# Optimization experiments

Measured on AMD Instinct MI355X. Metric: run time of the kernel, lower is better.

## Reference

```python
import jax, jax.numpy as jnp
import numpy as np

D_MODEL, HEADS, D_FF = 1024, 16, 4096
D_K = D_MODEL // HEADS
EPS = 1e-5


def layer_norm(x, g, b):
    mu = jnp.mean(x, axis=-1, keepdims=True)
    var = jnp.mean((x - mu) ** 2, axis=-1, keepdims=True)
    return (x - mu) * jax.lax.rsqrt(var + EPS) * g + b


def setup_inputs() -> dict:
    key = jax.random.key(0)
    ks = jax.random.split(key, 16)
    B, S = 2, 2048
    s = 0.02
    return {
        "src": jax.random.normal(ks[0], (B, S, D_MODEL), jnp.float32),
        "corr": jax.random.normal(ks[1], (B, S, S), jnp.float32),
        "pos": jax.random.normal(ks[2], (B, S, D_MODEL), jnp.float32),
        "Wq": jax.random.normal(ks[3], (D_MODEL, D_MODEL), jnp.float32) * s,
        "bq": jnp.zeros((D_MODEL,), jnp.float32),
        "Wk": jax.random.normal(ks[4], (D_MODEL, D_MODEL), jnp.float32) * s,
        "bk": jnp.zeros((D_MODEL,), jnp.float32),
        "Wv": jax.random.normal(ks[5], (D_MODEL, D_MODEL), jnp.float32) * s,
        "bv": jnp.zeros((D_MODEL,), jnp.float32),
        "Wo": jax.random.normal(ks[6], (D_MODEL, D_MODEL), jnp.float32) * s,
        "bo": jnp.zeros((D_MODEL,), jnp.float32),
        "W1": jax.random.normal(ks[7], (D_MODEL, D_FF), jnp.float32) * s,
        "b1": jnp.zeros((D_FF,), jnp.float32),
        "W2": jax.random.normal(ks[8], (D_FF, D_MODEL), jnp.float32) * s,
        "b2": jnp.zeros((D_MODEL,), jnp.float32),
        "g1": jnp.ones((D_MODEL,), jnp.float32),
        "be1": jnp.zeros((D_MODEL,), jnp.float32),
        "g2": jnp.ones((D_MODEL,), jnp.float32),
        "be2": jnp.zeros((D_MODEL,), jnp.float32),
    }


def reference(src, corr, pos, Wq, bq, Wk, bk, Wv, bv, Wo, bo, W1, b1, W2, b2, g1, be1, g2, be2):
    B, S, _ = src.shape
    qk_in = src + pos  # with_pos_embed for q and k; value uses raw src
    # QKV projections -> [B, H, S, d_k]
    def split_heads(x):
        return x.reshape(B, S, HEADS, D_K).transpose(0, 2, 1, 3)
    q = split_heads(qk_in @ Wq + bq)
    k = split_heads(qk_in @ Wk + bk)
    v = split_heads(src @ Wv + bv)
    # scores [B, H, S, S] with additive correlation bias before softmax
    scores = jnp.einsum("bhqd,bhkd->bhqk", q, k) / jnp.sqrt(jnp.float32(D_K))
    scores = scores + corr[:, None, :, :]
    attn = jax.nn.softmax(scores, axis=-1)
    ctx = jnp.einsum("bhqk,bhkd->bhqd", attn, v)
    concat = ctx.transpose(0, 2, 1, 3).reshape(B, S, D_MODEL)
    attn_out = concat @ Wo + bo
    # post-norm residual blocks (dropout = identity in eval)
    x = layer_norm(src + attn_out, g1, be1)
    ffn = jax.nn.relu(x @ W1 + b1) @ W2 + b2
    x = layer_norm(x + ffn, g2, be2)
    return x
```

## Files before the change

kernel.cpp:

```cpp
#include <hip/hip_runtime.h>
#include <hip/hip_bf16.h>

#define S_LEN  2048
#define BATCH  2
#define DMODEL 1024
#define NHEAD  16
#define DHEAD  64
#define DFF    4096
#define NTOK   (BATCH * S_LEN)
#define QKVLD  3072
#define NSPLIT 2

typedef __attribute__((ext_vector_type(8))) short short8;
typedef __attribute__((ext_vector_type(4))) short short4v;
typedef __attribute__((ext_vector_type(4))) float f32x4;

__device__ __forceinline__ short f2bs(float f) {
  __hip_bfloat16 h = __float2bfloat16(f);
  short s;
  __builtin_memcpy(&s, &h, sizeof(short));
  return s;
}

__device__ __forceinline__ float bs2f(short s) {
  unsigned u = ((unsigned)(unsigned short)s) << 16;
  float f;
  __builtin_memcpy(&f, &u, sizeof(float));
  return f;
}

__device__ __forceinline__ f32x4 mfma16(short8 a, short8 b, f32x4 c) {
  return __builtin_amdgcn_mfma_f32_16x16x32_bf16(a, b, c, 0, 0, 0);
}

__device__ __forceinline__ void load_lds16(const short* g, short* l) {
  __builtin_amdgcn_global_load_lds(
      (const __attribute__((address_space(1))) void*)g,
      (__attribute__((address_space(3))) void*)l, 16, 0, 0);
}

__global__ void transpose_cast(const float* __restrict__ in, short* __restrict__ out,
                               int R, int C, float scale) {
  __shared__ float tile[32][33];
  const int c0 = blockIdx.x * 32, r0 = blockIdx.y * 32;
  const int tx = threadIdx.x, ty = threadIdx.y;
#pragma unroll
  for (int i = 0; i < 32; i += 8)
    tile[ty + i][tx] = in[(size_t)(r0 + ty + i) * C + c0 + tx];
  __syncthreads();
#pragma unroll
  for (int i = 0; i < 32; i += 8)
    out[(size_t)(c0 + ty + i) * R + r0 + tx] = f2bs(tile[tx][ty + i] * scale);
}

__global__ __launch_bounds__(256) void transpose_bf16(
    const short* __restrict__ in, short* __restrict__ out, int R, int LDin) {
  __shared__ __attribute__((aligned(16))) short tile[64][72];
  const int c0 = blockIdx.x * 64, r0 = blockIdx.y * 64;
#pragma unroll
  for (int i = 0; i < 2; i++) {
    const int idx = threadIdx.x + 256 * i;
    const int rr = idx >> 3, cc8 = (idx & 7) * 8;
    *(int4*)(&tile[rr][cc8]) = *(const int4*)(in + (size_t)(r0 + rr) * LDin + c0 + cc8);
  }
  __syncthreads();
#pragma unroll
  for (int i = 0; i < 2; i++) {
    const int idx = threadIdx.x + 256 * i;
    const int rr = idx >> 3, cc8 = (idx & 7) * 8;
    short8 v;
#pragma unroll
    for (int j = 0; j < 8; j++) v[j] = tile[cc8 + j][rr];
    *(short8*)(out + (size_t)(c0 + rr) * R + r0 + cc8) = v;
  }
}

__global__ void concat_bias(const float* __restrict__ bq, const float* __restrict__ bk,
                            const float* __restrict__ bv, float* __restrict__ bqkv) {
  const int i = blockIdx.x * 256 + threadIdx.x;
  float v;
  if (i < DMODEL) v = bq[i] * 0.125f;
  else if (i < 2 * DMODEL) v = bk[i - DMODEL];
  else v = bv[i - 2 * DMODEL];
  bqkv[i] = v;
}

__global__ void prep_tokens(const float* __restrict__ src, const float* __restrict__ pos,
                            short* __restrict__ qkb, short* __restrict__ srcb) {
  const int i = (blockIdx.x * blockDim.x + threadIdx.x) * 4;
  float4 s = *(const float4*)(src + i);
  float4 p = *(const float4*)(pos + i);
  short4v q4 = {f2bs(s.x + p.x), f2bs(s.y + p.y), f2bs(s.z + p.z), f2bs(s.w + p.w)};
  short4v s4 = {f2bs(s.x), f2bs(s.y), f2bs(s.z), f2bs(s.w)};
  *(short4v*)(qkb + i) = q4;
  *(short4v*)(srcb + i) = s4;
}

__global__ void prep_corr(const float* __restrict__ corr, short* __restrict__ corrb) {
  const size_t i = ((size_t)blockIdx.x * 256 + threadIdx.x) * 4;
  float4 c = *(const float4*)(corr + i);
  short4v o = {f2bs(c.x), f2bs(c.y), f2bs(c.z), f2bs(c.w)};
  *(short4v*)(corrb + i) = o;
}

template <int RELU, int OUT_BF16>
__global__ __launch_bounds__(256) void gemm_bt(
    const short* __restrict__ A0, const short* __restrict__ A1,
    const short* __restrict__ Bt, const float* __restrict__ bias,
    float* __restrict__ Cf, short* __restrict__ Cb,
    int M, int N, int K, int splitcol) {
  __shared__ __attribute__((aligned(16))) short As[128 * 32];
  __shared__ __attribute__((aligned(16))) short Bs[128 * 32];

  const int tid = threadIdx.x;
  const int wave = tid >> 6, lane = tid & 63;
  const int lm = lane & 15, lq = lane >> 4;
  const int row0 = blockIdx.y * 128, col0 = blockIdx.x * 128;
  const int wr = (wave >> 1) * 64, wc = (wave & 1) * 64;

  const short* A = (col0 < splitcol) ? A0 : A1;
  const short* ag = A + (size_t)(row0 + wave * 32 + (lane >> 2)) * K + (lane & 3) * 8;
  const short* bg = Bt + (size_t)(col0 + wave * 32 + (lane >> 2)) * K + (lane & 3) * 8;
  short* asl = &As[wave * 32 * 32];
  short* bsl = &Bs[wave * 32 * 32];

  f32x4 acc[4][4];
#pragma unroll
  for (int i = 0; i < 4; i++)
#pragma unroll
    for (int j = 0; j < 4; j++) acc[i][j] = (f32x4){0.f, 0.f, 0.f, 0.f};

  for (int k0 = 0; k0 < K; k0 += 32) {
    load_lds16(ag + k0, asl);
    load_lds16(ag + (size_t)16 * K + k0, asl + 16 * 32);
    load_lds16(bg + k0, bsl);
    load_lds16(bg + (size_t)16 * K + k0, bsl + 16 * 32);
    __syncthreads();

    short8 af[4], bfr[4];
#pragma unroll
    for (int i = 0; i < 4; i++)
      af[i] = *(const short8*)(&As[(wr + 16 * i + lm) * 32 + lq * 8]);
#pragma unroll
    for (int j = 0; j < 4; j++)
      bfr[j] = *(const short8*)(&Bs[(wc + 16 * j + lm) * 32 + lq * 8]);
#pragma unroll
    for (int i = 0; i < 4; i++)
#pragma unroll
      for (int j = 0; j < 4; j++) acc[i][j] = mfma16(af[i], bfr[j], acc[i][j]);
    __syncthreads();
  }

#pragma unroll
  for (int i = 0; i < 4; i++) {
#pragma unroll
    for (int j = 0; j < 4; j++) {
      const int col = col0 + wc + 16 * j + lm;
      const float bs = bias[col];
#pragma unroll
      for (int r = 0; r < 4; r++) {
        const int row = row0 + wr + 16 * i + lq * 4 + r;
        float v = acc[i][j][r] + bs;
        if (RELU) v = fmaxf(v, 0.f);
        if (OUT_BF16)
          Cb[(size_t)row * N + col] = f2bs(v);
        else
          Cf[(size_t)row * N + col] = v;
      }
    }
  }
}

__global__ __launch_bounds__(256) void gemm_bt_part(
    const short* __restrict__ A, const short* __restrict__ Bt,
    float* __restrict__ Cf, int M, int N, int K, int Kslice) {
  __shared__ __attribute__((aligned(16))) short As[128 * 32];
  __shared__ __attribute__((aligned(16))) short Bs[128 * 32];

  const int tid = threadIdx.x;
  const int wave = tid >> 6, lane = tid & 63;
  const int lm = lane & 15, lq = lane >> 4;
  const int row0 = blockIdx.y * 128, col0 = blockIdx.x * 128;
  const int kbase = blockIdx.z * Kslice;
  const int wr = (wave >> 1) * 64, wc = (wave & 1) * 64;
  Cf += (size_t)blockIdx.z * M * N;

  const short* ag = A + (size_t)(row0 + wave * 32 + (lane >> 2)) * K + (lane & 3) * 8;
  const short* bg = Bt + (size_t)(col0 + wave * 32 + (lane >> 2)) * K + (lane & 3) * 8;
  short* asl = &As[wave * 32 * 32];
  short* bsl = &Bs[wave * 32 * 32];

  f32x4 acc[4][4];
#pragma unroll
  for (int i = 0; i < 4; i++)
#pragma unroll
    for (int j = 0; j < 4; j++) acc[i][j] = (f32x4){0.f, 0.f, 0.f, 0.f};

  for (int k0 = kbase; k0 < kbase + Kslice; k0 += 32) {
    load_lds16(ag + k0, asl);
    load_lds16(ag + (size_t)16 * K + k0, asl + 16 * 32);
    load_lds16(bg + k0, bsl);
    load_lds16(bg + (size_t)16 * K + k0, bsl + 16 * 32);
    __syncthreads();

    short8 af[4], bfr[4];
#pragma unroll
    for (int i = 0; i < 4; i++)
      af[i] = *(const short8*)(&As[(wr + 16 * i + lm) * 32 + lq * 8]);
#pragma unroll
    for (int j = 0; j < 4; j++)
      bfr[j] = *(const short8*)(&Bs[(wc + 16 * j + lm) * 32 + lq * 8]);
#pragma unroll
    for (int i = 0; i < 4; i++)
#pragma unroll
      for (int j = 0; j < 4; j++) acc[i][j] = mfma16(af[i], bfr[j], acc[i][j]);
    __syncthreads();
  }

#pragma unroll
  for (int i = 0; i < 4; i++) {
#pragma unroll
    for (int j = 0; j < 4; j++) {
      const int col = col0 + wc + 16 * j + lm;
#pragma unroll
      for (int r = 0; r < 4; r++) {
        const int row = row0 + wr + 16 * i + lq * 4 + r;
        Cf[(size_t)row * N + col] = acc[i][j][r];
      }
    }
  }
}

__global__ __launch_bounds__(512, 8) void attn_kernel(
    const short* __restrict__ QKV,
    const short* __restrict__ VT,
    const short* __restrict__ corrb,
    float* __restrict__ Op,
    float* __restrict__ lp) {
  const int h = blockIdx.x, qtile = blockIdx.y;
  const int b = blockIdx.z >> 1, split = blockIdx.z & 1;
  const int koff = split * (S_LEN / NSPLIT);
  const int tid = threadIdx.x;
  const int wave = tid >> 6, lane = tid & 63;
  const int lm = lane & 15, lq = lane >> 4;
  const int qb = qtile * 128 + wave * 16;
  const int fx = lm & 7;
  const int fy = (lm >> 1) & 3;

  __shared__ __attribute__((aligned(16))) short Ks[32 * 64];
  __shared__ __attribute__((aligned(16))) short Vs[64 * 32];
  __shared__ __attribute__((aligned(16))) short Ps[8 * 16 * 32];

  const short* q0 = QKV + (size_t)(b * S_LEN + qb + lm) * QKVLD + h * DHEAD;
  const short8 qA0 = *(const short8*)(q0 + lq * 8);
  const short8 qA1 = *(const short8*)(q0 + lq * 8 + 32);

  f32x4 oA[4];
#pragma unroll
  for (int t = 0; t < 4; t++) oA[t] = (f32x4){0.f, 0.f, 0.f, 0.f};
  f32x4 lacc = (f32x4){0.f, 0.f, 0.f, 0.f};

  const short* c0 = corrb + (size_t)(b * S_LEN + qb + lm) * S_LEN;

  const int st = tid & 255;
  const bool isK = tid < 256;
  short* sdst;
  const short* sgp;
  size_t sstep;
  if (isK) {
    const int krow = st >> 3, ku = st & 7;
    sdst = &Ks[krow * 64 + ((ku ^ (krow & 7)) * 8)];
    sgp = QKV + (size_t)(b * S_LEN + koff + krow) * QKVLD + DMODEL + h * DHEAD + ku * 8;
    sstep = (size_t)32 * QKVLD;
  } else {
    const int vrow = st >> 2, vu = st & 3;
    sdst = &Vs[vrow * 32 + ((vu ^ ((vrow >> 1) & 3)) * 8)];
    sgp = VT + (size_t)(h * DHEAD + vrow) * NTOK + b * S_LEN + koff + vu * 8;
    sstep = 32;
  }

  for (int kt = koff; kt < koff + S_LEN / NSPLIT; kt += 32) {
    *(int4*)sdst = *(const int4*)sgp;
    sgp += sstep;
    __syncthreads();

    f32x4 sv[2];
    __builtin_amdgcn_s_setprio(1);
#pragma unroll
    for (int t = 0; t < 2; t++) {
      const int rb = (t * 16 + lm) * 64;
      const short8 kf0 = *(const short8*)(&Ks[rb + (lq ^ fx) * 8]);
      const short8 kf1 = *(const short8*)(&Ks[rb + ((lq + 4) ^ fx) * 8]);
      f32x4 a = (f32x4){0.f, 0.f, 0.f, 0.f};
      a = mfma16(kf0, qA0, a);
      a = mfma16(kf1, qA1, a);
      sv[t] = a;
    }
    __builtin_amdgcn_s_setprio(0);

#pragma unroll
    for (int t = 0; t < 2; t++) {
      const short4v cr = *(const short4v*)(c0 + kt + t * 16 + lq * 4);
#pragma unroll
      for (int r = 0; r < 4; r++)
        sv[t][r] = __expf(sv[t][r] + bs2f(cr[r]));
      lacc += sv[t];
      short4v pA = {f2bs(sv[t][0]), f2bs(sv[t][1]), f2bs(sv[t][2]), f2bs(sv[t][3])};
      const int pu = ((2 * t + (lq >> 1)) ^ fy) * 8 + (lq & 1) * 4;
      *(short4v*)(&Ps[wave * 512 + lm * 32 + pu]) = pA;
    }

    const short8 pA0 = *(const short8*)(&Ps[wave * 512 + lm * 32 + (lq ^ fy) * 8]);
    __builtin_amdgcn_s_setprio(1);
#pragma unroll
    for (int t = 0; t < 4; t++) {
      const int vrb = (t * 16 + lm) * 32;
      const short8 vf0 = *(const short8*)(&Vs[vrb + (lq ^ fy) * 8]);
      oA[t] = mfma16(vf0, pA0, oA[t]);
    }
    __builtin_amdgcn_s_setprio(0);
    __syncthreads();
  }

  float lA = lacc[0] + lacc[1] + lacc[2] + lacc[3];
  lA += __shfl_xor(lA, 16);
  lA += __shfl_xor(lA, 32);
  if (lq == 0)
    lp[((size_t)split * NTOK + b * S_LEN + qb + lm) * NHEAD + h] = lA;
  float* opA = Op + (size_t)split * NTOK * DMODEL +
               (size_t)(b * S_LEN + qb + lm) * DMODEL + h * DHEAD;
#pragma unroll
  for (int t = 0; t < 4; t++)
    *(f32x4*)(opA + t * 16 + lq * 4) = oA[t];
}

__global__ __launch_bounds__(256) void combine_ctx(
    const float* __restrict__ Op, const float* __restrict__ lp,
    short* __restrict__ ctx) {
  const size_t idx = ((size_t)blockIdx.x * 256 + threadIdx.x) * 4;
  const int token = (int)(idx >> 10);
  const int d = (int)(idx & 1023);
  const int h = d >> 6;
  f32x4 o = (f32x4){0.f, 0.f, 0.f, 0.f};
  float l = 0.f;
#pragma unroll
  for (int s = 0; s < NSPLIT; s++) {
    o += *(const f32x4*)(Op + (size_t)s * NTOK * DMODEL + idx);
    l += lp[((size_t)s * NTOK + token) * NHEAD + h];
  }
  const float inv = 1.0f / l;
  short4v ov = {f2bs(o[0] * inv), f2bs(o[1] * inv),
                f2bs(o[2] * inv), f2bs(o[3] * inv)};
  *(short4v*)(ctx + idx) = ov;
}

__global__ __launch_bounds__(256) void residual_ln3(
    const float* __restrict__ xa, const float* __restrict__ p0,
    const float* __restrict__ p1, const float* __restrict__ bias,
    const float* __restrict__ g, const float* __restrict__ be,
    float* __restrict__ outf, short* __restrict__ outb) {
  const int row = blockIdx.x;
  const int t = threadIdx.x;
  const size_t base = (size_t)row * DMODEL + t * 4;
  float4 a = *(const float4*)(xa + base);
  f32x4 q0 = *(const f32x4*)(p0 + base);
  f32x4 q1 = *(const f32x4*)(p1 + base);
  f32x4 bb = *(const f32x4*)(bias + t * 4);
  const float v0 = a.x + q0[0] + q1[0] + bb[0];
  const float v1 = a.y + q0[1] + q1[1] + bb[1];
  const float v2 = a.z + q0[2] + q1[2] + bb[2];
  const float v3 = a.w + q0[3] + q1[3] + bb[3];
  float sum = v0 + v1 + v2 + v3;
  float sq = v0 * v0 + v1 * v1 + v2 * v2 + v3 * v3;
#pragma unroll
  for (int off = 1; off < 64; off <<= 1) {
    sum += __shfl_xor(sum, off);
    sq += __shfl_xor(sq, off);
  }
  __shared__ float ssum[4], ssq[4];
  const int wave = t >> 6;
  if ((t & 63) == 0) { ssum[wave] = sum; ssq[wave] = sq; }
  __syncthreads();
  sum = ssum[0] + ssum[1] + ssum[2] + ssum[3];
  sq = ssq[0] + ssq[1] + ssq[2] + ssq[3];
  const float mean = sum * (1.0f / DMODEL);
  const float var = sq * (1.0f / DMODEL) - mean * mean;
  const float rstd = rsqrtf(var + 1e-5f);
  float4 gv = *(const float4*)(g + t * 4);
  float4 bv = *(const float4*)(be + t * 4);
  const float o0 = (v0 - mean) * rstd * gv.x + bv.x;
  const float o1 = (v1 - mean) * rstd * gv.y + bv.y;
  const float o2 = (v2 - mean) * rstd * gv.z + bv.z;
  const float o3 = (v3 - mean) * rstd * gv.w + bv.w;
  if (outf) {
    float4 ov = {o0, o1, o2, o3};
    *(float4*)(outf + base) = ov;
  }
  if (outb) {
    short4v ob = {f2bs(o0), f2bs(o1), f2bs(o2), f2bs(o3)};
    *(short4v*)(outb + base) = ob;
  }
}

extern "C" void kernel_launch(void* const* d_in, const int* in_sizes, int n_in,
                              void* d_out, int out_size, void* d_ws, size_t ws_size,
                              hipStream_t stream) {
  const float* src = (const float*)d_in[0];
  const float* corr = (const float*)d_in[1];
  const float* pos = (const float*)d_in[2];
  const float* Wq = (const float*)d_in[3];
  const float* bq = (const float*)d_in[4];
  const float* Wk = (const float*)d_in[5];
  const float* bk = (const float*)d_in[6];
  const float* Wv = (const float*)d_in[7];
  const float* bv = (const float*)d_in[8];
  const float* Wo = (const float*)d_in[9];
  const float* bo = (const float*)d_in[10];
  const float* W1 = (const float*)d_in[11];
  const float* b1 = (const float*)d_in[12];
  const float* W2 = (const float*)d_in[13];
  const float* b2 = (const float*)d_in[14];
  const float* g1 = (const float*)d_in[15];
  const float* be1 = (const float*)d_in[16];
  const float* g2 = (const float*)d_in[17];
  const float* be2 = (const float*)d_in[18];
  float* out = (float*)d_out;

  char* ws = (char*)d_ws;
  size_t off = 0;
  auto alloc = [&](size_t bytes) {
    char* p = ws + off;
    off += (bytes + 255) & ~(size_t)255;
    return p;
  };
  short* WqkvT = (short*)alloc((size_t)QKVLD * DMODEL * 2);
  short* WoT = (short*)alloc((size_t)DMODEL * DMODEL * 2);
  short* W1T = (short*)alloc((size_t)DFF * DMODEL * 2);
  short* W2T = (short*)alloc((size_t)DMODEL * DFF * 2);
  float* bqkv = (float*)alloc((size_t)QKVLD * 4);
  short* qkb = (short*)alloc((size_t)NTOK * DMODEL * 2);
  short* srcb = (short*)alloc((size_t)NTOK * DMODEL * 2);
  short* QKVb = (short*)alloc((size_t)NTOK * QKVLD * 2);
  short* VTt = (short*)alloc((size_t)DMODEL * NTOK * 2);
  short* corrb = (short*)alloc((size_t)BATCH * S_LEN * S_LEN * 2);
  short* ctxb = (short*)alloc((size_t)NTOK * DMODEL * 2);
  float* lp = (float*)alloc((size_t)NSPLIT * NTOK * NHEAD * 4);
  float* Pp = (float*)alloc((size_t)2 * NTOK * DMODEL * 4);
  short* Hb = (short*)alloc((size_t)NTOK * DFF * 2);
  float* Op = Pp;
  float* x1f = (float*)alloc((size_t)NTOK * DMODEL * 4);
  short* x1b = (short*)alloc((size_t)NTOK * DMODEL * 2);

  const dim3 tb(32, 8);
  transpose_cast<<<dim3(32, 32), tb, 0, stream>>>(Wq, WqkvT, DMODEL, DMODEL, 0.125f);
  transpose_cast<<<dim3(32, 32), tb, 0, stream>>>(Wk, WqkvT + (size_t)DMODEL * DMODEL,
                                                  DMODEL, DMODEL, 1.0f);
  transpose_cast<<<dim3(32, 32), tb, 0, stream>>>(Wv, WqkvT + (size_t)2 * DMODEL * DMODEL,
                                                  DMODEL, DMODEL, 1.0f);
  transpose_cast<<<dim3(32, 32), tb, 0, stream>>>(Wo, WoT, DMODEL, DMODEL, 1.0f);
  transpose_cast<<<dim3(128, 32), tb, 0, stream>>>(W1, W1T, DMODEL, DFF, 1.0f);
  transpose_cast<<<dim3(32, 128), tb, 0, stream>>>(W2, W2T, DFF, DMODEL, 1.0f);
  concat_bias<<<QKVLD / 256, 256, 0, stream>>>(bq, bk, bv, bqkv);

  prep_tokens<<<(NTOK * DMODEL) / (256 * 4), 256, 0, stream>>>(src, pos, qkb, srcb);
  prep_corr<<<(BATCH * S_LEN * S_LEN) / (256 * 4), 256, 0, stream>>>(corr, corrb);

  gemm_bt<0, 1><<<dim3(QKVLD / 128, NTOK / 128), 256, 0, stream>>>(
      qkb, srcb, WqkvT, bqkv, nullptr, QKVb, NTOK, QKVLD, DMODEL, 2048);

  transpose_bf16<<<dim3(DMODEL / 64, NTOK / 64), 256, 0, stream>>>(
      QKVb + 2048, VTt, NTOK, QKVLD);

  attn_kernel<<<dim3(NHEAD, S_LEN / 128, BATCH * NSPLIT), 512, 0, stream>>>(
      QKVb, VTt, corrb, Op, lp);
  combine_ctx<<<(NTOK * DMODEL) / (256 * 4), 256, 0, stream>>>(Op, lp, ctxb);

  gemm_bt_part<<<dim3(DMODEL / 128, NTOK / 128, 2), 256, 0, stream>>>(
      ctxb, WoT, Pp, NTOK, DMODEL, DMODEL, DMODEL / 2);

  residual_ln3<<<NTOK, 256, 0, stream>>>(src, Pp, Pp + (size_t)NTOK * DMODEL,
                                         bo, g1, be1, x1f, x1b);

  gemm_bt<1, 1><<<dim3(DFF / 128, NTOK / 128), 256, 0, stream>>>(
      x1b, x1b, W1T, b1, nullptr, Hb, NTOK, DFF, DMODEL, 1 << 30);

  gemm_bt_part<<<dim3(DMODEL / 128, NTOK / 128, 2), 256, 0, stream>>>(
      Hb, W2T, Pp, NTOK, DMODEL, DFF, DFF / 2);

  residual_ln3<<<NTOK, 256, 0, stream>>>(x1f, Pp, Pp + (size_t)NTOK * DMODEL,
                                         b2, g2, be2, out, nullptr);
}
```

Before: 480.7 us.

## Drop split-K attention, fuse normalization into attention, merge prep kernels

Attention no longer splits the key range across two blocks. Each block now walks all 2048 keys and writes the normalized bf16 context directly, so the fp32 partial outputs and the combine_ctx kernel go away. The weight transposes and bias concat are merged into one launch, as are the token and corr casts, to cut launch overhead. The cost is half as many attention blocks (512 instead of 1024), which may leave the GPU less occupied, and each block runs a loop twice as long.

```diff
diff --git a/kernel.cpp b/kernel.cpp
--- a/kernel.cpp
+++ b/kernel.cpp
@@ -9,7 +9,6 @@
 #define DFF    4096
 #define NTOK   (BATCH * S_LEN)
 #define QKVLD  3072
-#define NSPLIT 2
 
 typedef __attribute__((ext_vector_type(8))) short short8;
 typedef __attribute__((ext_vector_type(4))) short short4v;
@@ -39,11 +38,48 @@
       (__attribute__((address_space(3))) void*)l, 16, 0, 0);
 }
 
-__global__ void transpose_cast(const float* __restrict__ in, short* __restrict__ out,
-                               int R, int C, float scale) {
+__global__ void prep_static(
+    const float* __restrict__ Wq, const float* __restrict__ Wk,
+    const float* __restrict__ Wv, const float* __restrict__ Wo,
+    const float* __restrict__ W1, const float* __restrict__ W2,
+    const float* __restrict__ bq, const float* __restrict__ bk,
+    const float* __restrict__ bv,
+    short* __restrict__ WqkvT, short* __restrict__ WoT,
+    short* __restrict__ W1T, short* __restrict__ W2T,
+    float* __restrict__ bqkv) {
+  const int gid = blockIdx.x;
+  const int tx = threadIdx.x, ty = threadIdx.y;
+
+  if (gid >= 12288) {
+    const int i = (gid - 12288) * 256 + ty * 32 + tx;
+    float v;
+    if (i < DMODEL) v = bq[i] * 0.125f;
+    else if (i < 2 * DMODEL) v = bk[i - DMODEL];
+    else v = bv[i - 2 * DMODEL];
+    bqkv[i] = v;
+    return;
+  }
+
+  const float* in;
+  short* out;
+  int R, C, t;
+  float scale = 1.0f;
+  if (gid < 4096) {
+    t = gid & 1023;
+    R = C = 1024;
+    if (gid < 1024)      { in = Wq; out = WqkvT;                 scale = 0.125f; }
+    else if (gid < 2048) { in = Wk; out = WqkvT + 1024 * 1024; }
+    else if (gid < 3072) { in = Wv; out = WqkvT + 2 * 1024 * 1024; }
+    else                 { in = Wo; out = WoT; }
+  } else if (gid < 8192) {
+    t = gid - 4096; in = W1; out = W1T; R = 1024; C = 4096;
+  } else {
+    t = gid - 8192; in = W2; out = W2T; R = 4096; C = 1024;
+  }
+  const int tpr = C >> 5;
+  const int c0 = (t % tpr) * 32, r0 = (t / tpr) * 32;
+
   __shared__ float tile[32][33];
-  const int c0 = blockIdx.x * 32, r0 = blockIdx.y * 32;
-  const int tx = threadIdx.x, ty = threadIdx.y;
 #pragma unroll
   for (int i = 0; i < 32; i += 8)
     tile[ty + i][tx] = in[(size_t)(r0 + ty + i) * C + c0 + tx];
@@ -51,6 +87,27 @@
 #pragma unroll
   for (int i = 0; i < 32; i += 8)
     out[(size_t)(c0 + ty + i) * R + r0 + tx] = f2bs(tile[tx][ty + i] * scale);
+}
+
+__global__ void prep_inputs(const float* __restrict__ src, const float* __restrict__ pos,
+                            const float* __restrict__ corr,
+                            short* __restrict__ qkb, short* __restrict__ srcb,
+                            short* __restrict__ corrb) {
+  const int gid = blockIdx.x;
+  if (gid < 4096) {
+    const int i = gid * 1024 + threadIdx.x * 4;
+    float4 s = *(const float4*)(src + i);
+    float4 p = *(const float4*)(pos + i);
+    short4v q4 = {f2bs(s.x + p.x), f2bs(s.y + p.y), f2bs(s.z + p.z), f2bs(s.w + p.w)};
+    short4v s4 = {f2bs(s.x), f2bs(s.y), f2bs(s.z), f2bs(s.w)};
+    *(short4v*)(qkb + i) = q4;
+    *(short4v*)(srcb + i) = s4;
+  } else {
+    const size_t i = ((size_t)(gid - 4096)) * 1024 + threadIdx.x * 4;
+    float4 c = *(const float4*)(corr + i);
+    short4v o = {f2bs(c.x), f2bs(c.y), f2bs(c.z), f2bs(c.w)};
+    *(short4v*)(corrb + i) = o;
+  }
 }
 
 __global__ __launch_bounds__(256) void transpose_bf16(
@@ -73,34 +130,6 @@
     for (int j = 0; j < 8; j++) v[j] = tile[cc8 + j][rr];
     *(short8*)(out + (size_t)(c0 + rr) * R + r0 + cc8) = v;
   }
-}
-
-__global__ void concat_bias(const float* __restrict__ bq, const float* __restrict__ bk,
-                            const float* __restrict__ bv, float* __restrict__ bqkv) {
-  const int i = blockIdx.x * 256 + threadIdx.x;
-  float v;
-  if (i < DMODEL) v = bq[i] * 0.125f;
-  else if (i < 2 * DMODEL) v = bk[i - DMODEL];
-  else v = bv[i - 2 * DMODEL];
-  bqkv[i] = v;
-}
-
-__global__ void prep_tokens(const float* __restrict__ src, const float* __restrict__ pos,
-                            short* __restrict__ qkb, short* __restrict__ srcb) {
-  const int i = (blockIdx.x * blockDim.x + threadIdx.x) * 4;
-  float4 s = *(const float4*)(src + i);
-  float4 p = *(const float4*)(pos + i);
-  short4v q4 = {f2bs(s.x + p.x), f2bs(s.y + p.y), f2bs(s.z + p.z), f2bs(s.w + p.w)};
-  short4v s4 = {f2bs(s.x), f2bs(s.y), f2bs(s.z), f2bs(s.w)};
-  *(short4v*)(qkb + i) = q4;
-  *(short4v*)(srcb + i) = s4;
-}
-
-__global__ void prep_corr(const float* __restrict__ corr, short* __restrict__ corrb) {
-  const size_t i = ((size_t)blockIdx.x * 256 + threadIdx.x) * 4;
-  float4 c = *(const float4*)(corr + i);
-  short4v o = {f2bs(c.x), f2bs(c.y), f2bs(c.z), f2bs(c.w)};
-  *(short4v*)(corrb + i) = o;
 }
 
 template <int RELU, int OUT_BF16>
@@ -235,11 +264,9 @@
     const short* __restrict__ QKV,
     const short* __restrict__ VT,
     const short* __restrict__ corrb,
-    float* __restrict__ Op,
-    float* __restrict__ lp) {
+    short* __restrict__ ctx) {
   const int h = blockIdx.x, qtile = blockIdx.y;
-  const int b = blockIdx.z >> 1, split = blockIdx.z & 1;
-  const int koff = split * (S_LEN / NSPLIT);
+  const int b = blockIdx.z;
   const int tid = threadIdx.x;
   const int wave = tid >> 6, lane = tid & 63;
   const int lm = lane & 15, lq = lane >> 4;
@@ -270,16 +297,16 @@
   if (isK) {
     const int krow = st >> 3, ku = st & 7;
     sdst = &Ks[krow * 64 + ((ku ^ (krow & 7)) * 8)];
-    sgp = QKV + (size_t)(b * S_LEN + koff + krow) * QKVLD + DMODEL + h * DHEAD + ku * 8;
+    sgp = QKV + (size_t)(b * S_LEN + krow) * QKVLD + DMODEL + h * DHEAD + ku * 8;
     sstep = (size_t)32 * QKVLD;
   } else {
     const int vrow = st >> 2, vu = st & 3;
     sdst = &Vs[vrow * 32 + ((vu ^ ((vrow >> 1) & 3)) * 8)];
-    sgp = VT + (size_t)(h * DHEAD + vrow) * NTOK + b * S_LEN + koff + vu * 8;
+    sgp = VT + (size_t)(h * DHEAD + vrow) * NTOK + b * S_LEN + vu * 8;
     sstep = 32;
   }
 
-  for (int kt = koff; kt < koff + S_LEN / NSPLIT; kt += 32) {
+  for (int kt = 0; kt < S_LEN; kt += 32) {
     *(int4*)sdst = *(const int4*)sgp;
     sgp += sstep;
     __syncthreads();
@@ -325,33 +352,14 @@
   float lA = lacc[0] + lacc[1] + lacc[2] + lacc[3];
   lA += __shfl_xor(lA, 16);
   lA += __shfl_xor(lA, 32);
-  if (lq == 0)
-    lp[((size_t)split * NTOK + b * S_LEN + qb + lm) * NHEAD + h] = lA;
-  float* opA = Op + (size_t)split * NTOK * DMODEL +
-               (size_t)(b * S_LEN + qb + lm) * DMODEL + h * DHEAD;
-#pragma unroll
-  for (int t = 0; t < 4; t++)
-    *(f32x4*)(opA + t * 16 + lq * 4) = oA[t];
-}
-
-__global__ __launch_bounds__(256) void combine_ctx(
-    const float* __restrict__ Op, const float* __restrict__ lp,
-    short* __restrict__ ctx) {
-  const size_t idx = ((size_t)blockIdx.x * 256 + threadIdx.x) * 4;
-  const int token = (int)(idx >> 10);
-  const int d = (int)(idx & 1023);
-  const int h = d >> 6;
-  f32x4 o = (f32x4){0.f, 0.f, 0.f, 0.f};
-  float l = 0.f;
-#pragma unroll
-  for (int s = 0; s < NSPLIT; s++) {
-    o += *(const f32x4*)(Op + (size_t)s * NTOK * DMODEL + idx);
-    l += lp[((size_t)s * NTOK + token) * NHEAD + h];
-  }
-  const float inv = 1.0f / l;
-  short4v ov = {f2bs(o[0] * inv), f2bs(o[1] * inv),
-                f2bs(o[2] * inv), f2bs(o[3] * inv)};
-  *(short4v*)(ctx + idx) = ov;
+  const float inv = 1.0f / lA;
+  short* op = ctx + (size_t)(b * S_LEN + qb + lm) * DMODEL + h * DHEAD;
+#pragma unroll
+  for (int t = 0; t < 4; t++) {
+    short4v ov = {f2bs(oA[t][0] * inv), f2bs(oA[t][1] * inv),
+                  f2bs(oA[t][2] * inv), f2bs(oA[t][3] * inv)};
+    *(short4v*)(op + t * 16 + lq * 4) = ov;
+  }
 }
 
 __global__ __launch_bounds__(256) void residual_ln3(
@@ -444,26 +452,15 @@
   short* VTt = (short*)alloc((size_t)DMODEL * NTOK * 2);
   short* corrb = (short*)alloc((size_t)BATCH * S_LEN * S_LEN * 2);
   short* ctxb = (short*)alloc((size_t)NTOK * DMODEL * 2);
-  float* lp = (float*)alloc((size_t)NSPLIT * NTOK * NHEAD * 4);
   float* Pp = (float*)alloc((size_t)2 * NTOK * DMODEL * 4);
   short* Hb = (short*)alloc((size_t)NTOK * DFF * 2);
-  float* Op = Pp;
   float* x1f = (float*)alloc((size_t)NTOK * DMODEL * 4);
   short* x1b = (short*)alloc((size_t)NTOK * DMODEL * 2);
 
-  const dim3 tb(32, 8);
-  transpose_cast<<<dim3(32, 32), tb, 0, stream>>>(Wq, WqkvT, DMODEL, DMODEL, 0.125f);
-  transpose_cast<<<dim3(32, 32), tb, 0, stream>>>(Wk, WqkvT + (size_t)DMODEL * DMODEL,
-                                                  DMODEL, DMODEL, 1.0f);
-  transpose_cast<<<dim3(32, 32), tb, 0, stream>>>(Wv, WqkvT + (size_t)2 * DMODEL * DMODEL,
-                                                  DMODEL, DMODEL, 1.0f);
-  transpose_cast<<<dim3(32, 32), tb, 0, stream>>>(Wo, WoT, DMODEL, DMODEL, 1.0f);
-  transpose_cast<<<dim3(128, 32), tb, 0, stream>>>(W1, W1T, DMODEL, DFF, 1.0f);
-  transpose_cast<<<dim3(32, 128), tb, 0, stream>>>(W2, W2T, DFF, DMODEL, 1.0f);
-  concat_bias<<<QKVLD / 256, 256, 0, stream>>>(bq, bk, bv, bqkv);
-
-  prep_tokens<<<(NTOK * DMODEL) / (256 * 4), 256, 0, stream>>>(src, pos, qkb, srcb);
-  prep_corr<<<(BATCH * S_LEN * S_LEN) / (256 * 4), 256, 0, stream>>>(corr, corrb);
+  prep_static<<<12300, dim3(32, 8), 0, stream>>>(
+      Wq, Wk, Wv, Wo, W1, W2, bq, bk, bv, WqkvT, WoT, W1T, W2T, bqkv);
+
+  prep_inputs<<<12288, 256, 0, stream>>>(src, pos, corr, qkb, srcb, corrb);
 
   gemm_bt<0, 1><<<dim3(QKVLD / 128, NTOK / 128), 256, 0, stream>>>(
       qkb, srcb, WqkvT, bqkv, nullptr, QKVb, NTOK, QKVLD, DMODEL, 2048);
@@ -471,9 +468,8 @@
   transpose_bf16<<<dim3(DMODEL / 64, NTOK / 64), 256, 0, stream>>>(
       QKVb + 2048, VTt, NTOK, QKVLD);
 
-  attn_kernel<<<dim3(NHEAD, S_LEN / 128, BATCH * NSPLIT), 512, 0, stream>>>(
-      QKVb, VTt, corrb, Op, lp);
-  combine_ctx<<<(NTOK * DMODEL) / (256 * 4), 256, 0, stream>>>(Op, lp, ctxb);
+  attn_kernel<<<dim3(NHEAD, S_LEN / 128, BATCH), 512, 0, stream>>>(
+      QKVb, VTt, corrb, ctxb);
 
   gemm_bt_part<<<dim3(DMODEL / 128, NTOK / 128, 2), 256, 0, stream>>>(
       ctxb, WoT, Pp, NTOK, DMODEL, DMODEL, DMODEL / 2);
```

Result: no change. 480.6 us (-0.0%).
